# Kernel optimization log

Hardware: AMD Instinct MI355X
Metric: run time of the kernel (lower is better)

Reference implementation:

```python
import jax, jax.numpy as jnp
import numpy as np

N, E = 4096, 65536
H = 200
KS = (3072, 1536, 768)  # ceil(0.75*4096), ceil(0.5*3072), ceil(0.5*1536)


def _gcn(A, x, W, b):
    # GCNConv with improved=True: A_hat = A + 2I, sym-normalized
    n = A.shape[0]
    Ah = A + 2.0 * jnp.eye(n, dtype=A.dtype)
    dinv = jax.lax.rsqrt(Ah.sum(axis=1))
    An = dinv[:, None] * Ah * dinv[None, :]
    return An @ (x @ W) + b


def _augment(A):
    # GraphUNet.augment_adj: remove self loops, add self loops (w=1), spspmm(A,A), remove self loops
    n = A.shape[0]
    eye = jnp.eye(n, dtype=A.dtype)
    Ap = A * (1.0 - eye) + eye
    A2 = Ap @ Ap  # dense form of spspmm (two-hop adjacency with weights)
    return A2 * (1.0 - eye)


def _pool(A, x, pw, k):
    # TopKPooling: score = tanh(x.w/||w||), keep top-k, scale kept x by score
    score = jnp.tanh((x @ pw) / jnp.linalg.norm(pw))
    val, perm = jax.lax.top_k(score, k)
    return x[perm] * val[:, None], A[perm][:, perm], perm


def _unet(x, adj, w0, b0, w1, b1, w2, b2, w3, b3, p1, p2, p3,
          u0w, u0b, u1w, u1b, u2w, u2b):
    down = [(w1, b1), (w2, b2), (w3, b3)]
    pws = [p1, p2, p3]
    up = [(u0w, u0b), (u1w, u1b), (u2w, u2b)]
    x = jax.nn.relu(_gcn(adj, x, w0, b0))
    xs, As, perms = [x], [adj], []
    A = adj
    for i in range(3):
        A = _augment(A)
        x, A, perm = _pool(A, x, pws[i], KS[i])
        x = jax.nn.relu(_gcn(A, x, *down[i]))
        if i < 2:
            xs.append(x)
            As.append(A)
        perms.append(perm)
    for i in range(3):
        j = 2 - i
        upf = jnp.zeros_like(xs[j]).at[perms[j]].set(x)
        x = xs[j] + upf  # sum_res=True
        x = _gcn(As[j], x, *up[i])
        if i < 2:
            x = jax.nn.relu(x)
    return jax.nn.log_softmax(x, axis=1)


def setup_inputs() -> dict:
    key = jax.random.key(0)
    ks = jax.random.split(key, 16)
    x = jax.random.normal(ks[0], (N, 3), dtype=jnp.float32)
    src = jax.random.randint(ks[1], (E,), 0, N)
    dst = jax.random.randint(ks[2], (E,), 0, N)
    A = jnp.zeros((N, N), jnp.float32).at[src, dst].set(1.0)
    A = jnp.maximum(A, A.T) * (1.0 - jnp.eye(N, dtype=jnp.float32))
    g = lambda k, s: jax.random.normal(k, s, jnp.float32) * 0.1
    z = lambda n: jnp.zeros((n,), jnp.float32)
    return dict(
        x=x, adj=A,
        w0=g(ks[3], (3, H)), b0=z(H),
        w1=g(ks[4], (H, H)), b1=z(H),
        w2=g(ks[5], (H, H)), b2=z(H),
        w3=g(ks[6], (H, H)), b3=z(H),
        p1=g(ks[7], (H,)), p2=g(ks[8], (H,)), p3=g(ks[9], (H,)),
        u0w=g(ks[10], (H, H)), u0b=z(H),
        u1w=g(ks[11], (H, H)), u1b=z(H),
        u2w=g(ks[12], (H, 2)), u2b=z(2),
    )


def reference(x, adj, w0, b0, w1, b1, w2, b2, w3, b3, p1, p2, p3,
              u0w, u0b, u1w, u1b, u2w, u2b):
    return _unet(x, adj, w0, b0, w1, b1, w2, b2, w3, b3, p1, p2, p3,
                 u0w, u0b, u1w, u1b, u2w, u2b)
```

## Files before the change

### kernel.cpp

```cpp
#include <hip/hip_runtime.h>

typedef unsigned short u16;
typedef unsigned int u32;
typedef unsigned long long u64;
typedef signed char s8;
typedef __attribute__((ext_vector_type(8))) short bfrag8;
typedef __attribute__((ext_vector_type(4))) float f32x4;
typedef __attribute__((ext_vector_type(4))) int i32x4;
typedef __attribute__((address_space(1))) const void gconst_void;
typedef __attribute__((address_space(3))) void lds_void_t;

__device__ __forceinline__ float bf2f(u16 u) {
  return __uint_as_float(((u32)u) << 16);
}
__device__ __forceinline__ u16 f2bf(float f) {
  u32 u = __float_as_uint(f);
  u32 r = (u + 0x7FFFu + ((u >> 16) & 1u)) >> 16;
  return (u16)r;
}
__device__ __forceinline__ void split3(float v, u16& hi, u16& mi, u16& lo) {
  hi = f2bf(v); float r1 = v - bf2f(hi);
  mi = f2bf(r1); float r2 = r1 - bf2f(mi);
  lo = f2bf(r2);
}
__device__ __forceinline__ float ld1(const void* p, int isbf, long idx) {
  return isbf ? bf2f(((const u16*)p)[idx]) : ((const float*)p)[idx];
}
__device__ __forceinline__ void ld4(const void* p, int isbf, long base, long gc, long bound, float v[4]) {
  if (gc + 3 < bound && ((base & 3) == 0)) {
    if (isbf) {
      const ushort4 u = *(const ushort4*)((const u16*)p + base);
      v[0] = bf2f(u.x); v[1] = bf2f(u.y); v[2] = bf2f(u.z); v[3] = bf2f(u.w);
    } else {
      const float4 f = *(const float4*)((const float*)p + base);
      v[0] = f.x; v[1] = f.y; v[2] = f.z; v[3] = f.w;
    }
  } else {
    #pragma unroll
    for (int d = 0; d < 4; ++d) v[d] = (gc + d < bound) ? ld1(p, isbf, base + d) : 0.f;
  }
}

__global__ void detect_k(const u32* __restrict__ a, long nw, int* __restrict__ flag) {
  long stride = (long)gridDim.x * 256;
  int f = 0;
  for (long j = (long)blockIdx.x * 256 + threadIdx.x; j < nw; j += stride) {
    u32 w = a[j];
    if (w == 0x00003F80u || w == 0x3F803F80u) f = 1;
  }
  if (__any(f)) {
    if ((threadIdx.x & 63) == 0) atomicOr(flag, 1);
  }
}

__device__ __forceinline__ int get_bf(int abf, const int* dtf) {
  return (abf >= 0) ? abf : *dtf;
}

__device__ __forceinline__ void stageB16(const void* g, void* lds) {
#if __has_builtin(__builtin_amdgcn_global_load_lds)
  __builtin_amdgcn_global_load_lds((gconst_void*)g, (lds_void_t*)lds, 16, 0, 0);
#else
  int lane = threadIdx.x & 63;
  *(int4*)((char*)lds + lane * 16) = *(const int4*)g;
#endif
}

template<typename PT>
__global__ __launch_bounds__(256) void syrk_tri_i8_parts(
    const s8* __restrict__ Ag, int ldk, int Ksplit, int ntri,
    PT* __restrict__ parts)
{
  __shared__ s8 At[2][128 * 64];
  __shared__ s8 Bt[2][128 * 64];
  const int t = blockIdx.x;
  int ti = (int)((sqrtf((float)(8 * t + 1)) - 1.0f) * 0.5f);
  while ((ti + 1) * (ti + 2) / 2 <= t) ++ti;
  while (ti * (ti + 1) / 2 > t) --ti;
  const int tj = t - ti * (ti + 1) / 2;

  const int tid = threadIdx.x;
  const int wave = tid >> 6, lane = tid & 63;
  const int wr = wave >> 1, wc = wave & 1;
  const long rowA0 = (long)ti * 128;
  const long rowB0 = (long)tj * 128;
  const int kbeg = blockIdx.y * Ksplit;
  const int nsteps = Ksplit / 64;

  i32x4 acc[4][4];
  #pragma unroll
  for (int i = 0; i < 4; ++i)
    #pragma unroll
    for (int j = 0; j < 4; ++j) acc[i][j] = (i32x4)0;

  const int srow = lane >> 2;
  const int scol = (lane & 3) * 16;
  const int m = lane & 15, q = lane >> 4;

  auto stage = [&](int buf, int k0) {
    #pragma unroll
    for (int tt = 0; tt < 2; ++tt) {
      const int r = wave * 32 + tt * 16;
      stageB16(Ag + (rowA0 + r + srow) * (long)ldk + k0 + scol, At[buf] + r * 64);
      stageB16(Ag + (rowB0 + r + srow) * (long)ldk + k0 + scol, Bt[buf] + r * 64);
    }
  };

  stage(0, kbeg);
  __syncthreads();
  int cur = 0;
  for (int st = 0; st < nsteps; ++st) {
    if (st + 1 < nsteps) stage(cur ^ 1, kbeg + (st + 1) * 64);

    i32x4 af[4], bf[4];
    #pragma unroll
    for (int mt = 0; mt < 4; ++mt)
      af[mt] = *(const i32x4*)(At[cur] + (wr * 64 + mt * 16 + m) * 64 + q * 16);
    #pragma unroll
    for (int nt = 0; nt < 4; ++nt)
      bf[nt] = *(const i32x4*)(Bt[cur] + (wc * 64 + nt * 16 + m) * 64 + q * 16);
    #pragma unroll
    for (int mt = 0; mt < 4; ++mt)
      #pragma unroll
      for (int nt = 0; nt < 4; ++nt)
        acc[mt][nt] = __builtin_amdgcn_mfma_i32_16x16x64_i8(af[mt], bf[nt], acc[mt][nt], 0, 0, 0);
    if (st + 1 < nsteps) __syncthreads();
    cur ^= 1;
  }

  PT* P = parts + ((long)blockIdx.y * ntri + t) * 16384;
  #pragma unroll
  for (int mt = 0; mt < 4; ++mt) {
    #pragma unroll
    for (int nt = 0; nt < 4; ++nt) {
      const int r0 = wr * 64 + mt * 16 + q * 4;
      const int c = wc * 64 + nt * 16 + m;
      #pragma unroll
      for (int r = 0; r < 4; ++r)
        P[(r0 + r) * 128 + c] = (PT)acc[mt][nt][r];
    }
  }
}

template<typename PT>
__global__ __launch_bounds__(256) void reduce_tri_i8_k(
    const PT* __restrict__ parts, int ntri, int n, int nz,
    u16* __restrict__ Ah, u16* __restrict__ Al, double* __restrict__ rs)
{
  __shared__ float T[128 * 33];
  const int t = blockIdx.x >> 2;
  const int slab = blockIdx.x & 3;
  int ti = (int)((sqrtf((float)(8 * t + 1)) - 1.0f) * 0.5f);
  while ((ti + 1) * (ti + 2) / 2 <= t) ++ti;
  while (ti * (ti + 1) / 2 > t) --ti;
  const int tj = t - ti * (ti + 1) / 2;
  const long rowA0 = (long)ti * 128;
  const long rowB0 = (long)tj * 128;
  const int r0 = slab * 32;
  const int tid = threadIdx.x;
  const int lane = tid & 63;
  const long tstride = (long)ntri * 16384;

  #pragma unroll
  for (int it = 0; it < 16; ++it) {
    const int idx = it * 256 + tid;
    const int lr = idx >> 7;
    const int lc = idx & 127;
    long base = (long)t * 16384 + (r0 + lr) * 128 + lc;
    int v = 0;
    for (int z = 0; z < nz; ++z) v += (int)parts[(long)z * tstride + base];
    const long gr = rowA0 + r0 + lr;
    const long gc = rowB0 + lc;
    if (gr == gc) v = 0;
    const float fv = (float)v;
    const u16 h = f2bf(fv);
    const long o = gr * n + gc;
    Ah[o] = h;
    if (Al) Al[o] = f2bf(fv - bf2f(h));
    T[lc * 33 + lr] = fv;
    float wsum = fv;
    #pragma unroll
    for (int off = 32; off > 0; off >>= 1) wsum += __shfl_down(wsum, off);
    if (lane == 0) atomicAdd(&rs[gr], (double)wsum);
  }
  if (ti == tj) return;
  __syncthreads();
  #pragma unroll
  for (int it = 0; it < 16; ++it) {
    const int idx = it * 256 + tid;
    const int mr = idx >> 5;
    const int mc = idx & 31;
    const float fv = T[mr * 33 + mc];
    const u16 h = f2bf(fv);
    const long o = (rowB0 + mr) * n + rowA0 + r0 + mc;
    Ah[o] = h;
    if (Al) Al[o] = f2bf(fv - bf2f(h));
    float ws = fv;
    #pragma unroll
    for (int off = 16; off > 0; off >>= 1) ws += __shfl_down(ws, off);
    if ((lane & 31) == 0) atomicAdd(&rs[rowB0 + mr], (double)ws);
  }
}

__global__ __launch_bounds__(256) void syrk_tri2_parts(
    const u16* __restrict__ Ah, const u16* __restrict__ Al, int ldk,
    float* __restrict__ parts, int n, int per)
{
  __shared__ u16 Ath[128 * 32];
  __shared__ u16 Bth[128 * 32];
  __shared__ u16 Atl[128 * 32];
  __shared__ u16 Btl[128 * 32];
  const int t = blockIdx.x;
  int ti = (int)((sqrtf((float)(8 * t + 1)) - 1.0f) * 0.5f);
  while ((ti + 1) * (ti + 2) / 2 <= t) ++ti;
  while (ti * (ti + 1) / 2 > t) --ti;
  const int tj = t - ti * (ti + 1) / 2;

  const int tid = threadIdx.x;
  const int wave = tid >> 6, lane = tid & 63;
  const int wr = wave >> 1, wc = wave & 1;
  const long rowA0 = (long)ti * 128;
  const long rowB0 = (long)tj * 128;
  const int kbeg = blockIdx.y * per;
  const int kend = kbeg + per;

  f32x4 acc[4][4];
  #pragma unroll
  for (int i = 0; i < 4; ++i)
    #pragma unroll
    for (int j = 0; j < 4; ++j) acc[i][j] = (f32x4)0.f;

  const int srow = lane >> 2;
  const int scol = (lane & 3) * 8;
  const int m = lane & 15, q = lane >> 4;

  for (int k0 = kbeg; k0 < kend; k0 += 32) {
    #pragma unroll
    for (int tt = 0; tt < 2; ++tt) {
      const int r = wave * 32 + tt * 16;
      stageB16(Ah + (rowA0 + r + srow) * (long)ldk + k0 + scol, Ath + r * 32);
      stageB16(Ah + (rowB0 + r + srow) * (long)ldk + k0 + scol, Bth + r * 32);
      stageB16(Al + (rowA0 + r + srow) * (long)ldk + k0 + scol, Atl + r * 32);
      stageB16(Al + (rowB0 + r + srow) * (long)ldk + k0 + scol, Btl + r * 32);
    }
    __syncthreads();

    bfrag8 afh[4], afl[4], bfh[4], bfl[4];
    #pragma unroll
    for (int mt = 0; mt < 4; ++mt) {
      afh[mt] = *(const bfrag8*)(Ath + (wr * 64 + mt * 16 + m) * 32 + q * 8);
      afl[mt] = *(const bfrag8*)(Atl + (wr * 64 + mt * 16 + m) * 32 + q * 8);
    }
    #pragma unroll
    for (int nt = 0; nt < 4; ++nt) {
      bfh[nt] = *(const bfrag8*)(Bth + (wc * 64 + nt * 16 + m) * 32 + q * 8);
      bfl[nt] = *(const bfrag8*)(Btl + (wc * 64 + nt * 16 + m) * 32 + q * 8);
    }
    #pragma unroll
    for (int mt = 0; mt < 4; ++mt)
      #pragma unroll
      for (int nt = 0; nt < 4; ++nt) {
        acc[mt][nt] = __builtin_amdgcn_mfma_f32_16x16x32_bf16(afh[mt], bfh[nt], acc[mt][nt], 0, 0, 0);
        acc[mt][nt] = __builtin_amdgcn_mfma_f32_16x16x32_bf16(afh[mt], bfl[nt], acc[mt][nt], 0, 0, 0);
        acc[mt][nt] = __builtin_amdgcn_mfma_f32_16x16x32_bf16(afl[mt], bfh[nt], acc[mt][nt], 0, 0, 0);
        acc[mt][nt] = __builtin_amdgcn_mfma_f32_16x16x32_bf16(afl[mt], bfl[nt], acc[mt][nt], 0, 0, 0);
      }
    __syncthreads();
  }

  float* P = parts + (long)blockIdx.y * n * n;
  #pragma unroll
  for (int mt = 0; mt < 4; ++mt) {
    #pragma unroll
    for (int nt = 0; nt < 4; ++nt) {
      const long gr0 = rowA0 + wr * 64 + mt * 16 + q * 4;
      const long gc = rowB0 + wc * 64 + nt * 16 + m;
      #pragma unroll
      for (int r = 0; r < 4; ++r)
        P[(gr0 + r) * n + gc] = acc[mt][nt][r];
    }
  }
}

__global__ void reduce_tri_mirror_k(const float* __restrict__ parts,
                                    u16* __restrict__ Ah, u16* __restrict__ Al,
                                    double* __restrict__ rsum, int n, int nz) {
  __shared__ double red[256];
  const int tid = threadIdx.x;
  long idx = (long)blockIdx.x * 256 + tid;
  long nn = (long)n * n;
  long r = idx / n, c = idx - r * n;
  double myv = 0.0;
  if (idx < nn) {
    if (r == c) {
      Ah[idx] = 0; Al[idx] = 0;
    } else if (r > c) {
      float s = 0.f;
      for (int z = 0; z < nz; ++z) s += parts[(long)z * nn + r * n + c];
      long mi = c * n + r;
      u16 h = f2bf(s);
      u16 l = f2bf(s - bf2f(h));
      Ah[idx] = h; Al[idx] = l;
      Ah[mi] = h;  Al[mi] = l;
      myv = (double)s;
      atomicAdd(&rsum[c], (double)s);
    }
  }
  red[tid] = myv;
  __syncthreads();
  for (int st = 128; st > 0; st >>= 1) {
    if (tid < st) red[tid] += red[tid + st];
    __syncthreads();
  }
  if (tid == 0 && idx < nn) atomicAdd(&rsum[r], red[0]);
}

__global__ void bg_i8_k(const void* __restrict__ src, int srcbf, int nsrc,
                        const int* __restrict__ perm, int kRows,
                        s8* __restrict__ Ag, const int* __restrict__ dtf,
                        const float* __restrict__ xsrc, const float* __restrict__ score,
                        float* __restrict__ xdst, unsigned nbB) {
  if (blockIdx.x < nbB) {
    long tot = (long)kRows * nsrc;
    long idx = (long)blockIdx.x * 256 + threadIdx.x;
    if (idx >= tot) return;
    int r = (int)(idx / nsrc);
    int c = (int)(idx - (long)r * nsrc);
    int p = perm[r];
    float v = ld1(src, get_bf(srcbf, dtf), (long)p * nsrc + c);
    if (c == p) v += 1.f;
    Ag[idx] = (s8)(int)v;
  } else {
    long tot = (long)kRows * 200;
    long idx = (long)(blockIdx.x - nbB) * 256 + threadIdx.x;
    if (idx >= tot) return;
    int r = (int)(idx / 200);
    int c = (int)(idx - (long)r * 200);
    int p = perm[r];
    xdst[idx] = xsrc[(long)p * 200 + c] * score[p];
  }
}

__global__ void bg_sp_k(const u16* __restrict__ srcH, const u16* __restrict__ srcL,
                        int nsrc, const int* __restrict__ perm, int kRows,
                        u16* __restrict__ Agh, u16* __restrict__ Agl,
                        const float* __restrict__ xsrc, const float* __restrict__ score,
                        float* __restrict__ xdst, unsigned nbB) {
  if (blockIdx.x < nbB) {
    long tot = (long)kRows * nsrc;
    long idx = (long)blockIdx.x * 256 + threadIdx.x;
    if (idx >= tot) return;
    int r = (int)(idx / nsrc);
    int c = (int)(idx - (long)r * nsrc);
    int p = perm[r];
    long si = (long)p * nsrc + c;
    float v = bf2f(srcH[si]) + bf2f(srcL[si]);
    if (c == p) v += 1.f;
    u16 h = f2bf(v);
    Agh[idx] = h;
    Agl[idx] = f2bf(v - bf2f(h));
  } else {
    long tot = (long)kRows * 200;
    long idx = (long)(blockIdx.x - nbB) * 256 + threadIdx.x;
    if (idx >= tot) return;
    int r = (int)(idx / 200);
    int c = (int)(idx - (long)r * 200);
    int p = perm[r];
    xdst[idx] = xsrc[(long)p * 200 + c] * score[p];
  }
}

template<int HASAL>
__global__ __launch_bounds__(512, 4) void agg_mfma8z(
    const u16* __restrict__ Ah, const u16* __restrict__ Al,
    const u16* __restrict__ ZT, float* __restrict__ parts,
    int K, int per_steps)
{
  __shared__ u16 At[2][8 * 512];
  __shared__ u16 Alt[HASAL ? 2 * 8 * 512 : 2];
  __shared__ u16 Zt[2][21 * 512];

  const int tid = threadIdx.x;
  const int wave = tid >> 6, lane = tid & 63;
  const int zh = blockIdx.z;
  const int ct0 = zh ? 7 : 0;
  const int nts = zh ? 6 : 7;
  const int cth = (nts + 1) >> 1;
  const int rg = wave & 3;
  const int cg = wave >> 2;
  const int wct0 = cg ? cth : 0;
  const int wnct = cg ? (nts - cth) : cth;
  const long row0 = (long)blockIdx.x * 128;
  const int chunk = blockIdx.y;
  const int kbeg = chunk * per_steps * 32;
  const int nsteps = (min(K, kbeg + per_steps * 32) - kbeg) / 32;
  const int m = lane & 15, q = lane >> 4;
  const int srow = lane >> 2, scol = (lane & 3) * 8;
  const int nstg = (HASAL ? 16 : 8) + 3 * nts;

  auto stage = [&](int buf, int k0) {
    for (int s = wave; s < nstg; s += 8) {
      if (s < 8) {
        stageB16(Ah + (row0 + s * 16 + srow) * (long)K + k0 + scol, At[buf] + s * 512);
      } else if (HASAL && s < 16) {
        stageB16(Al + (row0 + (s - 8) * 16 + srow) * (long)K + k0 + scol,
                 (u16*)Alt + (buf * 8 + (s - 8)) * 512);
      } else {
        const int zz = s - (HASAL ? 16 : 8);
        const int pl = (zz >= 2 * nts) ? 2 : ((zz >= nts) ? 1 : 0);
        const int c = zz - pl * nts;
        stageB16(ZT + ((long)(pl * 208 + (ct0 + c) * 16 + srow)) * K + k0 + scol,
                 Zt[buf] + (pl * 7 + c) * 512);
      }
    }
  };

  f32x4 acc[2][4];
  #pragma unroll
  for (int rt = 0; rt < 2; ++rt)
    #pragma unroll
    for (int ct = 0; ct < 4; ++ct) acc[rt][ct] = (f32x4)0.f;

  stage(0, kbeg);
  __syncthreads();
  int cur = 0;
  for (int t = 0; t < nsteps; ++t) {
    if (t + 1 < nsteps) stage(cur ^ 1, kbeg + (t + 1) * 32);

    const u16* Atb = At[cur];
    const u16* Ztb = Zt[cur];
    bfrag8 af0 = *(const bfrag8*)(Atb + (rg * 2) * 512 + m * 32 + q * 8);
    bfrag8 af1 = *(const bfrag8*)(Atb + (rg * 2 + 1) * 512 + m * 32 + q * 8);
    bfrag8 al0, al1;
    if (HASAL) {
      const u16* Altb = (const u16*)Alt + cur * 8 * 512;
      al0 = *(const bfrag8*)(Altb + (rg * 2) * 512 + m * 32 + q * 8);
      al1 = *(const bfrag8*)(Altb + (rg * 2 + 1) * 512 + m * 32 + q * 8);
    }
    #pragma unroll
    for (int ct = 0; ct < 4; ++ct) {
      if (ct < wnct) {
        const int gct = wct0 + ct;
        bfrag8 b0 = *(const bfrag8*)(Ztb + (0 * 7 + gct) * 512 + m * 32 + q * 8);
        bfrag8 b1 = *(const bfrag8*)(Ztb + (1 * 7 + gct) * 512 + m * 32 + q * 8);
        bfrag8 b2 = *(const bfrag8*)(Ztb + (2 * 7 + gct) * 512 + m * 32 + q * 8);
        acc[0][ct] = __builtin_amdgcn_mfma_f32_16x16x32_bf16(af0, b0, acc[0][ct], 0, 0, 0);
        acc[0][ct] = __builtin_amdgcn_mfma_f32_16x16x32_bf16(af0, b1, acc[0][ct], 0, 0, 0);
        acc[0][ct] = __builtin_amdgcn_mfma_f32_16x16x32_bf16(af0, b2, acc[0][ct], 0, 0, 0);
        acc[1][ct] = __builtin_amdgcn_mfma_f32_16x16x32_bf16(af1, b0, acc[1][ct], 0, 0, 0);
        acc[1][ct] = __builtin_amdgcn_mfma_f32_16x16x32_bf16(af1, b1, acc[1][ct], 0, 0, 0);
        acc[1][ct] = __builtin_amdgcn_mfma_f32_16x16x32_bf16(af1, b2, acc[1][ct], 0, 0, 0);
        if (HASAL) {
          acc[0][ct] = __builtin_amdgcn_mfma_f32_16x16x32_bf16(al0, b0, acc[0][ct], 0, 0, 0);
          acc[0][ct] = __builtin_amdgcn_mfma_f32_16x16x32_bf16(al0, b1, acc[0][ct], 0, 0, 0);
          acc[1][ct] = __builtin_amdgcn_mfma_f32_16x16x32_bf16(al1, b0, acc[1][ct], 0, 0, 0);
          acc[1][ct] = __builtin_amdgcn_mfma_f32_16x16x32_bf16(al1, b1, acc[1][ct], 0, 0, 0);
        }
      }
    }
    if (t + 1 < nsteps) __syncthreads();
    cur ^= 1;
  }

  float* P = parts + (long)chunk * gridDim.x * 128 * 208;
  #pragma unroll
  for (int rt = 0; rt < 2; ++rt) {
    #pragma unroll
    for (int ct = 0; ct < 4; ++ct) {
      if (ct < wnct) {
        const long grow0 = row0 + rg * 32 + rt * 16 + q * 4;
        const long gcol = (ct0 + wct0 + ct) * 16 + m;
        #pragma unroll
        for (int r = 0; r < 4; ++r)
          P[(grow0 + r) * 208 + gcol] = acc[rt][ct][r];
      }
    }
  }
}

__global__ __launch_bounds__(256) void reduce_epi_k(
    const float* __restrict__ parts, const float* __restrict__ Zs,
    const double* __restrict__ rs, const float* __restrict__ b,
    float* __restrict__ out, int n, int nz, int relu,
    const float* __restrict__ pw, float* __restrict__ score)
{
  __shared__ float vrow[200];
  const int i = blockIdx.x, tid = threadIdx.x;
  float dv = (float)(1.0 / sqrt(rs[i] + 2.0));
  if (tid < 200) {
    long base = (long)i * 208 + tid;
    float s = 0.f;
    for (int c = 0; c < nz; ++c) s += parts[(long)c * n * 208 + base];
    float v = dv * (s + 2.f * Zs[(long)i * 200 + tid]) + b[tid];
    if (relu) v = fmaxf(v, 0.f);
    out[(long)i * 200 + tid] = v;
    if (score) vrow[tid] = v;
  }
  if (!score) return;
  __syncthreads();
  if (tid < 64) {
    double ps = 0.0;
    for (int j = tid; j < 200; j += 64) { double w = pw[j]; ps += w * w; }
    for (int off = 32; off > 0; off >>= 1) ps += __shfl_down(ps, off);
    double nrm = sqrt(__shfl(ps, 0));
    double s = 0.0;
    for (int j = tid; j < 200; j += 64) s += (double)vrow[j] * (double)pw[j];
    for (int off = 32; off > 0; off >>= 1) s += __shfl_down(s, off);
    if (tid == 0) score[i] = (float)tanh(s / nrm);
  }
}

__global__ void a_from_adj_rs_k(const void* __restrict__ adj, const int* __restrict__ dtf,
                                int n, u16* __restrict__ Ah, double* __restrict__ rs) {
  __shared__ double red[256];
  int bf = *dtf;
  const int row = blockIdx.x, tid = threadIdx.x;
  const long base = (long)row * n;
  double s = 0.0;
  for (int j = tid; j < n; j += 256) {
    float v = ld1(adj, bf, base + j);
    Ah[base + j] = bf ? ((const u16*)adj)[base + j] : f2bf(v);
    s += (double)v;
  }
  red[tid] = s; __syncthreads();
  for (int st = 128; st > 0; st >>= 1) {
    if (tid < st) red[tid] += red[tid + st];
    __syncthreads();
  }
  if (tid == 0) rs[row] = red[0];
}

__global__ __launch_bounds__(256) void gemm64_f64(
    const void* __restrict__ Ap, long lda, int abf,
    const void* __restrict__ Bp, long ldb, int bbf,
    float* __restrict__ C, long ldc, int M, int N, int K,
    const double* __restrict__ rsum, u16* __restrict__ ZT, const int* __restrict__ dtf)
{
  const int abf_ = get_bf(abf, dtf);
  const int bbf_ = get_bf(bbf, dtf);
  __shared__ float As[16][64];
  __shared__ float Bs[16][64];
  const int tid = threadIdx.x;
  const int tr = tid >> 4, tc = tid & 15;
  const long row0 = (long)blockIdx.y * 64;
  const long col0 = (long)blockIdx.x * 64;
  double acc[4][4];
  #pragma unroll
  for (int i = 0; i < 4; ++i)
    #pragma unroll
    for (int j = 0; j < 4; ++j) acc[i][j] = 0.0;

  const int am = tid >> 2;
  const int ak = (tid & 3) * 4;
  const int bk = tid >> 4;
  const int bn = (tid & 15) * 4;

  for (int k0 = 0; k0 < K; k0 += 16) {
    float va[4] = {0.f, 0.f, 0.f, 0.f};
    {
      long gm = row0 + am; long gk = k0 + ak;
      if (gm < M && gk < K) ld4(Ap, abf_, gm * lda + gk, gk, K, va);
    }
    As[ak + 0][am] = va[0]; As[ak + 1][am] = va[1];
    As[ak + 2][am] = va[2]; As[ak + 3][am] = va[3];

    float vb[4] = {0.f, 0.f, 0.f, 0.f};
    {
      long gk = k0 + bk; long gn = col0 + bn;
      if (gk < K && gn < N) ld4(Bp, bbf_, gk * ldb + gn, gn, N, vb);
    }
    Bs[bk][bn + 0] = vb[0]; Bs[bk][bn + 1] = vb[1];
    Bs[bk][bn + 2] = vb[2]; Bs[bk][bn + 3] = vb[3];

    __syncthreads();
    #pragma unroll
    for (int kk = 0; kk < 16; ++kk) {
      float a[4], b[4];
      #pragma unroll
      for (int i = 0; i < 4; ++i) a[i] = As[kk][tr * 4 + i];
      #pragma unroll
      for (int j = 0; j < 4; ++j) b[j] = Bs[kk][tc * 4 + j];
      #pragma unroll
      for (int i = 0; i < 4; ++i)
        #pragma unroll
        for (int j = 0; j < 4; ++j)
          acc[i][j] += (double)a[i] * (double)b[j];
    }
    __syncthreads();
  }
  #pragma unroll
  for (int i = 0; i < 4; ++i) {
    long gm = row0 + tr * 4 + i;
    if (gm >= M) continue;
    float sc = rsum ? (float)(1.0 / sqrt(rsum[gm] + 2.0)) : 1.f;
    #pragma unroll
    for (int j = 0; j < 4; ++j) {
      long gn = col0 + tc * 4 + j;
      if (gn < N) {
        float v0 = (float)acc[i][j];
        float v = v0 * sc;
        C[gm * ldc + gn] = v;
        if (ZT) {
          u16 hi, mi, lo; split3(v, hi, mi, lo);
          ZT[((long)0 * 208 + gn) * M + gm] = hi;
          ZT[((long)1 * 208 + gn) * M + gm] = mi;
          ZT[((long)2 * 208 + gn) * M + gm] = lo;
        }
      }
    }
  }
}

struct UpBatch {
  const void* src[19];
  float* dst[19];
  int n[19];
};

__global__ void upcast_batch_k(UpBatch ub, const int* __restrict__ dtf) {
  int bf = *dtf;
  int a = blockIdx.y;
  int i = blockIdx.x * 256 + threadIdx.x;
  if (i < ub.n[a]) ub.dst[a][i] = ld1(ub.src[a], bf, i);
}

__global__ __launch_bounds__(256) void rank_part_k(
    const float* __restrict__ score, int n, int ns, int* __restrict__ prank)
{
  __shared__ u64 sk[256];
  const int tid = threadIdx.x;
  const int s = blockIdx.x;
  const int slice = n / ns;
  const int jb = s * slice;
  for (int j = tid; j < slice; j += 256) {
    int gj = jb + j;
    u32 b = __float_as_uint(score[gj]);
    u32 u = (b & 0x80000000u) ? ~b : (b | 0x80000000u);
    sk[j] = ((u64)u << 32) | (u32)(~(u32)gj);
  }
  __syncthreads();
  const int i0 = tid * 16;
  if (i0 >= n) return;
  u64 myk[16];
  int cnt[16];
  #pragma unroll
  for (int e = 0; e < 16; ++e) {
    int i = i0 + e;
    u64 key = 0ULL;
    if (i < n) {
      u32 b = __float_as_uint(score[i]);
      u32 u = (b & 0x80000000u) ? ~b : (b | 0x80000000u);
      key = ((u64)u << 32) | (u32)(~(u32)i);
    }
    myk[e] = key; cnt[e] = 0;
  }
  #pragma unroll 4
  for (int j = 0; j < slice; ++j) {
    u64 kj = sk[j];
    #pragma unroll
    for (int e = 0; e < 16; ++e) cnt[e] += (kj > myk[e]) ? 1 : 0;
  }
  #pragma unroll
  for (int e = 0; e < 16; ++e) {
    int i = i0 + e;
    if (i < n) prank[s * n + i] = cnt[e];
  }
}

__global__ void rank_scatter_k(const int* __restrict__ prank, int n, int ns, int k,
                               int* __restrict__ perm, int* __restrict__ inv) {
  int i = blockIdx.x * 256 + threadIdx.x;
  if (i >= n) return;
  int r = 0;
  for (int s = 0; s < ns; ++s) r += prank[s * n + i];
  inv[i] = (r < k) ? r : -1;
  if (r < k) perm[r] = i;
}

__global__ void upadd_k(const float* __restrict__ xs, const float* __restrict__ xpool,
                        const int* __restrict__ inv, float* __restrict__ dst, long nh, int h) {
  long idx = (long)blockIdx.x * 256 + threadIdx.x;
  if (idx >= nh) return;
  int i = (int)(idx / h);
  int c = (int)(idx - (long)i * h);
  float v = xs[idx];
  int r = inv[i];
  if (r >= 0) v += xpool[(long)r * h + c];
  dst[idx] = v;
}

__global__ void matvec2_final_k(const void* __restrict__ A, int abf, int n,
                                const float* __restrict__ Zs, const double* __restrict__ rs0,
                                const float* __restrict__ b2, float* __restrict__ out,
                                const int* __restrict__ dtf) {
  const int bf = get_bf(abf, dtf);
  int row = blockIdx.x, tid = threadIdx.x;
  const long base = (long)row * n;
  double s0 = 0.0, s1 = 0.0;
  for (int j = tid; j < n; j += 256) {
    double a = (double)ld1(A, bf, base + j);
    s0 += a * (double)Zs[2 * j];
    s1 += a * (double)Zs[2 * j + 1];
  }
  __shared__ double r0[256], r1[256];
  r0[tid] = s0; r1[tid] = s1; __syncthreads();
  for (int st = 128; st > 0; st >>= 1) {
    if (tid < st) { r0[tid] += r0[tid + st]; r1[tid] += r1[tid + st]; }
    __syncthreads();
  }
  if (tid == 0) {
    double y0 = (double)((float)r0[0]);
    double y1 = (double)((float)r1[0]);
    double di = (double)((float)(1.0 / sqrt(rs0[row] + 2.0)));
    double t0 = di * (y0 + 2.0 * (double)Zs[2 * row]) + (double)b2[0];
    double t1 = di * (y1 + 2.0 * (double)Zs[2 * row + 1]) + (double)b2[1];
    double mx = fmax(t0, t1);
    double l = mx + log(exp(t0 - mx) + exp(t1 - mx));
    out[2 * row] = (float)(t0 - l);
    out[2 * row + 1] = (float)(t1 - l);
  }
}

extern "C" void kernel_launch(void* const* d_in, const int* in_sizes, int n_in,
                              void* d_out, int out_size, void* d_ws, size_t ws_size,
                              hipStream_t stream) {
  const int N0 = 4096, H = 200;
  const int K1 = 3072, K2 = 1536, K3 = 768;
  const int TK_NS = 32;

  const void* in_x = d_in[0];
  const void* adj  = d_in[1];
  const void* w0 = d_in[2];  const void* b0 = d_in[3];
  const void* w1 = d_in[4];  const void* b1 = d_in[5];
  const void* w2 = d_in[6];  const void* b2 = d_in[7];
  const void* w3 = d_in[8];  const void* b3 = d_in[9];
  const void* p1 = d_in[10]; const void* p2 = d_in[11];
  const void* p3 = d_in[12];
  const void* u0w = d_in[13]; const void* u0b = d_in[14];
  const void* u1w = d_in[15]; const void* u1b = d_in[16];
  const void* u2w = d_in[17]; const void* u2b = d_in[18];

  char* wp = (char*)d_ws;
  auto alloc = [&](size_t bytes) -> void* {
    void* p = (void*)wp;
    wp += (bytes + 255) & ~(size_t)255;
    return p;
  };
  size_t partsBytes = (size_t)300 * 4 * 16384 * 4 + 1024;
  float* parts = (float*)alloc(partsBytes);
  s8*    Agb  = (s8*)alloc((size_t)K1 * N0);
  u16* Ag3h = (u16*)alloc((size_t)K3 * K2 * 2);
  u16* Ag3l = (u16*)alloc((size_t)K3 * K2 * 2);
  u16* Ah0 = (u16*)alloc((size_t)N0 * N0 * 2);
  u16* Ah1 = (u16*)alloc((size_t)K1 * K1 * 2);
  u16* Ah2 = (u16*)alloc((size_t)K2 * K2 * 2);
  u16* Al2 = (u16*)alloc((size_t)K2 * K2 * 2);
  u16* Ah3 = (u16*)alloc((size_t)K3 * K3 * 2);
  u16* Al3 = (u16*)alloc((size_t)K3 * K3 * 2);
  u16* ZT  = (u16*)alloc((size_t)3 * 208 * N0 * 2);
  float* xs0  = (float*)alloc((size_t)N0 * H * 4);
  float* xs1  = (float*)alloc((size_t)K1 * H * 4);
  float* xs2  = (float*)alloc((size_t)K2 * H * 4);
  float* xcur = (float*)alloc((size_t)N0 * H * 4);
  float* xtmp = (float*)alloc((size_t)N0 * H * 4);
  float* Zbuf = (float*)alloc((size_t)N0 * H * 4);
  float* Xinf = (float*)alloc((size_t)N0 * 3 * 4);
  double* rs0 = (double*)alloc((size_t)N0 * 8);
  double* rs1 = (double*)alloc((size_t)K1 * 8);
  double* rs2 = (double*)alloc((size_t)K2 * 8);
  double* rs3 = (double*)alloc((size_t)K3 * 8);
  int* dtflag = (int*)alloc(256);
  float* scores = (float*)alloc((size_t)N0 * 4);
  int* prank = (int*)alloc((size_t)TK_NS * N0 * 4);
  int* perm1 = (int*)alloc((size_t)K1 * 4);
  int* perm2 = (int*)alloc((size_t)K2 * 4);
  int* perm3 = (int*)alloc((size_t)K3 * 4);
  int* inv1 = (int*)alloc((size_t)N0 * 4);
  int* inv2 = (int*)alloc((size_t)K1 * 4);
  int* inv3 = (int*)alloc((size_t)K2 * 4);
  float* w0f = (float*)alloc(3 * H * 4);  float* b0f = (float*)alloc(H * 4);
  float* w1f = (float*)alloc(H * H * 4);  float* b1f = (float*)alloc(H * 4);
  float* w2f = (float*)alloc(H * H * 4);  float* b2f = (float*)alloc(H * 4);
  float* w3f = (float*)alloc(H * H * 4);  float* b3f = (float*)alloc(H * 4);
  float* p1f = (float*)alloc(H * 4);
  float* p2f = (float*)alloc(H * 4);
  float* p3f = (float*)alloc(H * 4);
  float* u0wf = (float*)alloc(H * H * 4); float* u0bf = (float*)alloc(H * 4);
  float* u1wf = (float*)alloc(H * H * 4); float* u1bf = (float*)alloc(H * 4);
  float* u2wf = (float*)alloc(H * 2 * 4); float* u2bf = (float*)alloc(2 * 4);
  (void)in_sizes; (void)n_in; (void)out_size; (void)ws_size;

  hipMemsetAsync(rs1, 0, (size_t)(K1 + K2 + K3) * 8 + 256, stream);
  detect_k<<<dim3(4096), dim3(256), 0, stream>>>((const u32*)adj, (long)N0 * N0 / 2, dtflag);

  {
    UpBatch ub;
    const void* srcs[19] = {in_x, w0, b0, w1, b1, w2, b2, w3, b3, p1, p2, p3,
                            u0w, u0b, u1w, u1b, u2w, u2b, u2b};
    float* dsts[19] = {Xinf, w0f, b0f, w1f, b1f, w2f, b2f, w3f, b3f, p1f, p2f, p3f,
                       u0wf, u0bf, u1wf, u1bf, u2wf, u2bf, u2bf};
    int ns[19] = {N0 * 3, 3 * H, H, H * H, H, H * H, H, H * H, H, H, H, H,
                  H * H, H, H * H, H, H * 2, 2, 2};
    for (int i = 0; i < 19; ++i) { ub.src[i] = srcs[i]; ub.dst[i] = dsts[i]; ub.n[i] = ns[i]; }
    upcast_batch_k<<<dim3((N0 * 3 + 255) / 256, 19), dim3(256), 0, stream>>>(ub, dtflag);
  }

  a_from_adj_rs_k<<<dim3(N0), dim3(256), 0, stream>>>(adj, dtflag, N0, Ah0, rs0);

  auto gemm64 = [&](const void* A, long lda, int abf, const void* B, long ldb, int bbf,
                    float* C, long ldc, int M, int Nn, int K, const double* rsum, u16* zt) {
    dim3 g((Nn + 63) / 64, (M + 63) / 64);
    gemm64_f64<<<g, dim3(256), 0, stream>>>(A, lda, abf, B, ldb, bbf, C, ldc, M, Nn, K,
                                            rsum, zt, dtflag);
  };

  auto gcn = [&](const u16* Ah, const u16* Al, int n, int chunks, const double* rs,
                 const float* Xin_, int din, const float* W, const float* bb,
                 float* out, const float* pwf, float* scoreOut) {
    gemm64(Xin_, din, 0, W, H, 0, Zbuf, H, n, H, din, rs, ZT);
    if (Al)
      agg_mfma8z<1><<<dim3(n / 128, chunks, 2), dim3(512), 0, stream>>>(
          Ah, Al, ZT, parts, n, (n / 32) / chunks);
    else
      agg_mfma8z<0><<<dim3(n / 128, chunks, 2), dim3(512), 0, stream>>>(
          Ah, nullptr, ZT, parts, n, (n / 32) / chunks);
    reduce_epi_k<<<dim3(n), dim3(256), 0, stream>>>(
        parts, Zbuf, rs, bb, out, n, chunks, 1, pwf, scoreOut);
  };

  auto topk = [&](const float* sc, int n, int k, int* perm, int* inv) {
    rank_part_k<<<dim3(TK_NS), dim3(256), 0, stream>>>(sc, n, TK_NS, prank);
    rank_scatter_k<<<dim3((unsigned)((n + 255) / 256)), dim3(256), 0, stream>>>(
        prank, n, TK_NS, k, perm, inv);
  };

  gcn(Ah0, nullptr, N0, 8, rs0, Xinf, 3, w0f, b0f, xs0, p1f, scores);

  topk(scores, N0, K1, perm1, inv1);
  {
    unsigned nbB = (unsigned)(((long)K1 * N0 + 255) / 256);
    unsigned nbG = (unsigned)(((long)K1 * 200 + 255) / 256);
    bg_i8_k<<<dim3(nbB + nbG), dim3(256), 0, stream>>>(
        adj, -1, N0, perm1, K1, Agb, dtflag, xs0, scores, xcur, nbB);
    int nt = K1 / 128;
    int ntri = nt * (nt + 1) / 2;
    syrk_tri_i8_parts<short><<<dim3(ntri, 4), dim3(256), 0, stream>>>(
        Agb, N0, N0 / 4, ntri, (short*)parts);
    reduce_tri_i8_k<short><<<dim3(ntri * 4), dim3(256), 0, stream>>>(
        (const short*)parts, ntri, K1, 4, Ah1, nullptr, rs1);
  }
  gcn(Ah1, nullptr, K1, 12, rs1, xcur, H, w1f, b1f, xs1, p2f, scores);

  topk(scores, K1, K2, perm2, inv2);
  {
    unsigned nbB = (unsigned)(((long)K2 * K1 + 255) / 256);
    unsigned nbG = (unsigned)(((long)K2 * 200 + 255) / 256);
    bg_i8_k<<<dim3(nbB + nbG), dim3(256), 0, stream>>>(
        Ah1, 1, K1, perm2, K2, Agb, dtflag, xs1, scores, xcur, nbB);
    int nt = K2 / 128;
    int ntri = nt * (nt + 1) / 2;
    syrk_tri_i8_parts<int><<<dim3(ntri, 8), dim3(256), 0, stream>>>(
        Agb, K1, K1 / 8, ntri, (int*)parts);
    reduce_tri_i8_k<int><<<dim3(ntri * 4), dim3(256), 0, stream>>>(
        (const int*)parts, ntri, K2, 8, Ah2, Al2, rs2);
  }
  gcn(Ah2, Al2, K2, 24, rs2, xcur, H, w2f, b2f, xs2, p3f, scores);

  topk(scores, K2, K3, perm3, inv3);
  {
    unsigned nbB = (unsigned)(((long)K3 * K2 + 255) / 256);
    unsigned nbG = (unsigned)(((long)K3 * 200 + 255) / 256);
    bg_sp_k<<<dim3(nbB + nbG), dim3(256), 0, stream>>>(
        Ah2, Al2, K2, perm3, K3, Ag3h, Ag3l, xs2, scores, xcur, nbB);
    int nt = K3 / 128;
    syrk_tri2_parts<<<dim3(nt * (nt + 1) / 2, 8), dim3(256), 0, stream>>>(
        Ag3h, Ag3l, K2, parts, K3, K2 / 8);
    long nn = (long)K3 * K3;
    reduce_tri_mirror_k<<<dim3((unsigned)(nn / 256)), dim3(256), 0, stream>>>(
        parts, Ah3, Al3, rs3, K3, 8);
  }
  gcn(Ah3, Al3, K3, 24, rs3, xcur, H, w3f, b3f, xcur, nullptr, nullptr);

  upadd_k<<<dim3((unsigned)(((long)K2 * H + 255) / 256)), dim3(256), 0, stream>>>(
      xs2, xcur, inv3, xtmp, (long)K2 * H, H);
  gcn(Ah2, Al2, K2, 24, rs2, xtmp, H, u0wf, u0bf, xcur, nullptr, nullptr);

  upadd_k<<<dim3((unsigned)(((long)K1 * H + 255) / 256)), dim3(256), 0, stream>>>(
      xs1, xcur, inv2, xtmp, (long)K1 * H, H);
  gcn(Ah1, nullptr, K1, 12, rs1, xtmp, H, u1wf, u1bf, xcur, nullptr, nullptr);

  upadd_k<<<dim3((unsigned)(((long)N0 * H + 255) / 256)), dim3(256), 0, stream>>>(
      xs0, xcur, inv1, xtmp, (long)N0 * H, H);
  gemm64(xtmp, H, 0, u2wf, 2, 0, Zbuf, 2, N0, 2, H, rs0, nullptr);
  matvec2_final_k<<<dim3(N0), dim3(256), 0, stream>>>(
      adj, -1, N0, Zbuf, rs0, u2bf, (float*)d_out, dtflag);
}
```

Before: 823.7 us.

## Vectorize gather kernels, double-buffer syrk_tri2, fuse unpool-add into GEMM loads

Converts several elementwise kernels (dtype detection, adjacency gather, row-sum copy, final matvec) to 4- or 8-wide vector loads and stores to cut instruction and memory-transaction overhead. It adds LDS double-buffering to the bf16 split SYRK so the next k-slice loads while MFMAs run, at the cost of doubled shared memory. It also removes the separate unpool-add kernels by folding the skip-plus-scattered-pool add into the GEMM A-operand load, which saves a round trip through a temporary buffer. The vector paths assume row lengths are multiples of four or eight and that buffers are suitably aligned.

```diff
diff --git a/kernel.cpp b/kernel.cpp
--- a/kernel.cpp
+++ b/kernel.cpp
@@ -42,11 +42,15 @@
 }
 
 __global__ void detect_k(const u32* __restrict__ a, long nw, int* __restrict__ flag) {
+  long nv = nw >> 2;
   long stride = (long)gridDim.x * 256;
   int f = 0;
-  for (long j = (long)blockIdx.x * 256 + threadIdx.x; j < nw; j += stride) {
-    u32 w = a[j];
-    if (w == 0x00003F80u || w == 0x3F803F80u) f = 1;
+  for (long j = (long)blockIdx.x * 256 + threadIdx.x; j < nv; j += stride) {
+    uint4 w = ((const uint4*)a)[j];
+    if (w.x == 0x00003F80u || w.x == 0x3F803F80u ||
+        w.y == 0x00003F80u || w.y == 0x3F803F80u ||
+        w.z == 0x00003F80u || w.z == 0x3F803F80u ||
+        w.w == 0x00003F80u || w.w == 0x3F803F80u) f = 1;
   }
   if (__any(f)) {
     if ((threadIdx.x & 63) == 0) atomicOr(flag, 1);
@@ -206,10 +210,10 @@
     const u16* __restrict__ Ah, const u16* __restrict__ Al, int ldk,
     float* __restrict__ parts, int n, int per)
 {
-  __shared__ u16 Ath[128 * 32];
-  __shared__ u16 Bth[128 * 32];
-  __shared__ u16 Atl[128 * 32];
-  __shared__ u16 Btl[128 * 32];
+  __shared__ u16 Ath[2][128 * 32];
+  __shared__ u16 Bth[2][128 * 32];
+  __shared__ u16 Atl[2][128 * 32];
+  __shared__ u16 Btl[2][128 * 32];
   const int t = blockIdx.x;
   int ti = (int)((sqrtf((float)(8 * t + 1)) - 1.0f) * 0.5f);
   while ((ti + 1) * (ti + 2) / 2 <= t) ++ti;
@@ -222,7 +226,7 @@
   const long rowA0 = (long)ti * 128;
   const long rowB0 = (long)tj * 128;
   const int kbeg = blockIdx.y * per;
-  const int kend = kbeg + per;
+  const int nsteps = per / 32;
 
   f32x4 acc[4][4];
   #pragma unroll
@@ -234,27 +238,33 @@
   const int scol = (lane & 3) * 8;
   const int m = lane & 15, q = lane >> 4;
 
-  for (int k0 = kbeg; k0 < kend; k0 += 32) {
+  auto stage = [&](int buf, int k0) {
     #pragma unroll
     for (int tt = 0; tt < 2; ++tt) {
       const int r = wave * 32 + tt * 16;
-      stageB16(Ah + (rowA0 + r + srow) * (long)ldk + k0 + scol, Ath + r * 32);
-      stageB16(Ah + (rowB0 + r + srow) * (long)ldk + k0 + scol, Bth + r * 32);
-      stageB16(Al + (rowA0 + r + srow) * (long)ldk + k0 + scol, Atl + r * 32);
-      stageB16(Al + (rowB0 + r + srow) * (long)ldk + k0 + scol, Btl + r * 32);
-    }
-    __syncthreads();
+      stageB16(Ah + (rowA0 + r + srow) * (long)ldk + k0 + scol, Ath[buf] + r * 32);
+      stageB16(Ah + (rowB0 + r + srow) * (long)ldk + k0 + scol, Bth[buf] + r * 32);
+      stageB16(Al + (rowA0 + r + srow) * (long)ldk + k0 + scol, Atl[buf] + r * 32);
+      stageB16(Al + (rowB0 + r + srow) * (long)ldk + k0 + scol, Btl[buf] + r * 32);
+    }
+  };
+
+  stage(0, kbeg);
+  __syncthreads();
+  int cur = 0;
+  for (int st = 0; st < nsteps; ++st) {
+    if (st + 1 < nsteps) stage(cur ^ 1, kbeg + (st + 1) * 32);
 
     bfrag8 afh[4], afl[4], bfh[4], bfl[4];
     #pragma unroll
     for (int mt = 0; mt < 4; ++mt) {
-      afh[mt] = *(const bfrag8*)(Ath + (wr * 64 + mt * 16 + m) * 32 + q * 8);
-      afl[mt] = *(const bfrag8*)(Atl + (wr * 64 + mt * 16 + m) * 32 + q * 8);
+      afh[mt] = *(const bfrag8*)(Ath[cur] + (wr * 64 + mt * 16 + m) * 32 + q * 8);
+      afl[mt] = *(const bfrag8*)(Atl[cur] + (wr * 64 + mt * 16 + m) * 32 + q * 8);
     }
     #pragma unroll
     for (int nt = 0; nt < 4; ++nt) {
-      bfh[nt] = *(const bfrag8*)(Bth + (wc * 64 + nt * 16 + m) * 32 + q * 8);
-      bfl[nt] = *(const bfrag8*)(Btl + (wc * 64 + nt * 16 + m) * 32 + q * 8);
+      bfh[nt] = *(const bfrag8*)(Bth[cur] + (wc * 64 + nt * 16 + m) * 32 + q * 8);
+      bfl[nt] = *(const bfrag8*)(Btl[cur] + (wc * 64 + nt * 16 + m) * 32 + q * 8);
     }
     #pragma unroll
     for (int mt = 0; mt < 4; ++mt)
@@ -265,7 +275,8 @@
         acc[mt][nt] = __builtin_amdgcn_mfma_f32_16x16x32_bf16(afl[mt], bfh[nt], acc[mt][nt], 0, 0, 0);
         acc[mt][nt] = __builtin_amdgcn_mfma_f32_16x16x32_bf16(afl[mt], bfl[nt], acc[mt][nt], 0, 0, 0);
       }
-    __syncthreads();
+    if (st + 1 < nsteps) __syncthreads();
+    cur ^= 1;
   }
 
   float* P = parts + (long)blockIdx.y * n * n;
@@ -321,23 +332,39 @@
                         const float* __restrict__ xsrc, const float* __restrict__ score,
                         float* __restrict__ xdst, unsigned nbB) {
   if (blockIdx.x < nbB) {
-    long tot = (long)kRows * nsrc;
-    long idx = (long)blockIdx.x * 256 + threadIdx.x;
-    if (idx >= tot) return;
+    long tot4 = ((long)kRows * nsrc) >> 2;
+    long i4 = (long)blockIdx.x * 256 + threadIdx.x;
+    if (i4 >= tot4) return;
+    long idx = i4 << 2;
     int r = (int)(idx / nsrc);
     int c = (int)(idx - (long)r * nsrc);
     int p = perm[r];
-    float v = ld1(src, get_bf(srcbf, dtf), (long)p * nsrc + c);
-    if (c == p) v += 1.f;
-    Ag[idx] = (s8)(int)v;
+    float v[4];
+    if (get_bf(srcbf, dtf)) {
+      ushort4 u = *(const ushort4*)((const u16*)src + (long)p * nsrc + c);
+      v[0] = bf2f(u.x); v[1] = bf2f(u.y); v[2] = bf2f(u.z); v[3] = bf2f(u.w);
+    } else {
+      float4 f = *(const float4*)((const float*)src + (long)p * nsrc + c);
+      v[0] = f.x; v[1] = f.y; v[2] = f.z; v[3] = f.w;
+    }
+    char4 o;
+    o.x = (s8)(int)(v[0] + ((c + 0 == p) ? 1.f : 0.f));
+    o.y = (s8)(int)(v[1] + ((c + 1 == p) ? 1.f : 0.f));
+    o.z = (s8)(int)(v[2] + ((c + 2 == p) ? 1.f : 0.f));
+    o.w = (s8)(int)(v[3] + ((c + 3 == p) ? 1.f : 0.f));
+    *(char4*)(Ag + idx) = o;
   } else {
-    long tot = (long)kRows * 200;
-    long idx = (long)(blockIdx.x - nbB) * 256 + threadIdx.x;
-    if (idx >= tot) return;
+    long tot4 = (long)kRows * 50;
+    long i4 = (long)(blockIdx.x - nbB) * 256 + threadIdx.x;
+    if (i4 >= tot4) return;
+    long idx = i4 << 2;
     int r = (int)(idx / 200);
     int c = (int)(idx - (long)r * 200);
     int p = perm[r];
-    xdst[idx] = xsrc[(long)p * 200 + c] * score[p];
+    float4 x = *(const float4*)(xsrc + (long)p * 200 + c);
+    float sc = score[p];
+    x.x *= sc; x.y *= sc; x.z *= sc; x.w *= sc;
+    *(float4*)(xdst + idx) = x;
   }
 }
 
@@ -347,26 +374,47 @@
                         const float* __restrict__ xsrc, const float* __restrict__ score,
                         float* __restrict__ xdst, unsigned nbB) {
   if (blockIdx.x < nbB) {
-    long tot = (long)kRows * nsrc;
-    long idx = (long)blockIdx.x * 256 + threadIdx.x;
-    if (idx >= tot) return;
+    long tot4 = ((long)kRows * nsrc) >> 2;
+    long i4 = (long)blockIdx.x * 256 + threadIdx.x;
+    if (i4 >= tot4) return;
+    long idx = i4 << 2;
     int r = (int)(idx / nsrc);
     int c = (int)(idx - (long)r * nsrc);
     int p = perm[r];
     long si = (long)p * nsrc + c;
-    float v = bf2f(srcH[si]) + bf2f(srcL[si]);
-    if (c == p) v += 1.f;
-    u16 h = f2bf(v);
-    Agh[idx] = h;
-    Agl[idx] = f2bf(v - bf2f(h));
+    ushort4 uh = *(const ushort4*)(srcH + si);
+    ushort4 ul = *(const ushort4*)(srcL + si);
+    ushort4 oh, ol;
+    {
+      float v = bf2f(uh.x) + bf2f(ul.x); if (c + 0 == p) v += 1.f;
+      oh.x = f2bf(v); ol.x = f2bf(v - bf2f(oh.x));
+    }
+    {
+      float v = bf2f(uh.y) + bf2f(ul.y); if (c + 1 == p) v += 1.f;
+      oh.y = f2bf(v); ol.y = f2bf(v - bf2f(oh.y));
+    }
+    {
+      float v = bf2f(uh.z) + bf2f(ul.z); if (c + 2 == p) v += 1.f;
+      oh.z = f2bf(v); ol.z = f2bf(v - bf2f(oh.z));
+    }
+    {
+      float v = bf2f(uh.w) + bf2f(ul.w); if (c + 3 == p) v += 1.f;
+      oh.w = f2bf(v); ol.w = f2bf(v - bf2f(oh.w));
+    }
+    *(ushort4*)(Agh + idx) = oh;
+    *(ushort4*)(Agl + idx) = ol;
   } else {
-    long tot = (long)kRows * 200;
-    long idx = (long)(blockIdx.x - nbB) * 256 + threadIdx.x;
-    if (idx >= tot) return;
+    long tot4 = (long)kRows * 50;
+    long i4 = (long)(blockIdx.x - nbB) * 256 + threadIdx.x;
+    if (i4 >= tot4) return;
+    long idx = i4 << 2;
     int r = (int)(idx / 200);
     int c = (int)(idx - (long)r * 200);
     int p = perm[r];
-    xdst[idx] = xsrc[(long)p * 200 + c] * score[p];
+    float4 x = *(const float4*)(xsrc + (long)p * 200 + c);
+    float sc = score[p];
+    x.x *= sc; x.y *= sc; x.z *= sc; x.w *= sc;
+    *(float4*)(xdst + idx) = x;
   }
 }
 
@@ -517,10 +565,27 @@
   const int row = blockIdx.x, tid = threadIdx.x;
   const long base = (long)row * n;
   double s = 0.0;
-  for (int j = tid; j < n; j += 256) {
-    float v = ld1(adj, bf, base + j);
-    Ah[base + j] = bf ? ((const u16*)adj)[base + j] : f2bf(v);
-    s += (double)v;
+  if (bf) {
+    const uint4* src = (const uint4*)((const u16*)adj + base);
+    uint4* dst = (uint4*)(Ah + base);
+    for (int j = tid; j < (n >> 3); j += 256) {
+      uint4 v = src[j];
+      dst[j] = v;
+      s += (double)(bf2f((u16)(v.x & 0xFFFFu)) + bf2f((u16)(v.x >> 16))
+                  + bf2f((u16)(v.y & 0xFFFFu)) + bf2f((u16)(v.y >> 16))
+                  + bf2f((u16)(v.z & 0xFFFFu)) + bf2f((u16)(v.z >> 16))
+                  + bf2f((u16)(v.w & 0xFFFFu)) + bf2f((u16)(v.w >> 16)));
+    }
+  } else {
+    const float4* src = (const float4*)((const float*)adj + base);
+    ushort4* dst = (ushort4*)(Ah + base);
+    for (int j = tid; j < (n >> 2); j += 256) {
+      float4 v = src[j];
+      ushort4 o;
+      o.x = f2bf(v.x); o.y = f2bf(v.y); o.z = f2bf(v.z); o.w = f2bf(v.w);
+      dst[j] = o;
+      s += (double)(v.x + v.y + v.z + v.w);
+    }
   }
   red[tid] = s; __syncthreads();
   for (int st = 128; st > 0; st >>= 1) {
@@ -534,7 +599,8 @@
     const void* __restrict__ Ap, long lda, int abf,
     const void* __restrict__ Bp, long ldb, int bbf,
     float* __restrict__ C, long ldc, int M, int N, int K,
-    const double* __restrict__ rsum, u16* __restrict__ ZT, const int* __restrict__ dtf)
+    const double* __restrict__ rsum, u16* __restrict__ ZT, const int* __restrict__ dtf,
+    const float* __restrict__ ua_pool, const int* __restrict__ ua_inv)
 {
   const int abf_ = get_bf(abf, dtf);
   const int bbf_ = get_bf(bbf, dtf);
@@ -554,12 +620,25 @@
   const int ak = (tid & 3) * 4;
   const int bk = tid >> 4;
   const int bn = (tid & 15) * 4;
+  const long gmA = row0 + am;
+  const int uar = (ua_inv && gmA < M) ? ua_inv[gmA] : -1;
 
   for (int k0 = 0; k0 < K; k0 += 16) {
     float va[4] = {0.f, 0.f, 0.f, 0.f};
     {
       long gm = row0 + am; long gk = k0 + ak;
-      if (gm < M && gk < K) ld4(Ap, abf_, gm * lda + gk, gk, K, va);
+      if (gm < M && gk < K) {
+        if (ua_inv) {
+          float4 x = *(const float4*)((const float*)Ap + gm * lda + gk);
+          if (uar >= 0) {
+            const float4 pv = *(const float4*)(ua_pool + (long)uar * lda + gk);
+            x.x += pv.x; x.y += pv.y; x.z += pv.z; x.w += pv.w;
+          }
+          va[0] = x.x; va[1] = x.y; va[2] = x.z; va[3] = x.w;
+        } else {
+          ld4(Ap, abf_, gm * lda + gk, gk, K, va);
+        }
+      }
     }
     As[ak + 0][am] = va[0]; As[ak + 1][am] = va[1];
     As[ak + 2][am] = va[2]; As[ak + 3][am] = va[3];
@@ -677,18 +756,6 @@
   if (r < k) perm[r] = i;
 }
 
-__global__ void upadd_k(const float* __restrict__ xs, const float* __restrict__ xpool,
-                        const int* __restrict__ inv, float* __restrict__ dst, long nh, int h) {
-  long idx = (long)blockIdx.x * 256 + threadIdx.x;
-  if (idx >= nh) return;
-  int i = (int)(idx / h);
-  int c = (int)(idx - (long)i * h);
-  float v = xs[idx];
-  int r = inv[i];
-  if (r >= 0) v += xpool[(long)r * h + c];
-  dst[idx] = v;
-}
-
 __global__ void matvec2_final_k(const void* __restrict__ A, int abf, int n,
                                 const float* __restrict__ Zs, const double* __restrict__ rs0,
                                 const float* __restrict__ b2, float* __restrict__ out,
@@ -697,10 +764,22 @@
   int row = blockIdx.x, tid = threadIdx.x;
   const long base = (long)row * n;
   double s0 = 0.0, s1 = 0.0;
-  for (int j = tid; j < n; j += 256) {
-    double a = (double)ld1(A, bf, base + j);
-    s0 += a * (double)Zs[2 * j];
-    s1 += a * (double)Zs[2 * j + 1];
+  for (int j4 = tid; j4 < (n >> 2); j4 += 256) {
+    const int j = j4 << 2;
+    float a0, a1, a2, a3;
+    if (bf) {
+      ushort4 u = *(const ushort4*)((const u16*)A + base + j);
+      a0 = bf2f(u.x); a1 = bf2f(u.y); a2 = bf2f(u.z); a3 = bf2f(u.w);
+    } else {
+      float4 f = *(const float4*)((const float*)A + base + j);
+      a0 = f.x; a1 = f.y; a2 = f.z; a3 = f.w;
+    }
+    const float4 z01 = *(const float4*)(Zs + 2 * j);
+    const float4 z23 = *(const float4*)(Zs + 2 * j + 4);
+    s0 += (double)a0 * (double)z01.x; s1 += (double)a0 * (double)z01.y;
+    s0 += (double)a1 * (double)z01.z; s1 += (double)a1 * (double)z01.w;
+    s0 += (double)a2 * (double)z23.x; s1 += (double)a2 * (double)z23.y;
+    s0 += (double)a3 * (double)z23.z; s1 += (double)a3 * (double)z23.w;
   }
   __shared__ double r0[256], r1[256];
   r0[tid] = s0; r1[tid] = s1; __syncthreads();
@@ -788,10 +867,10 @@
   float* u0wf = (float*)alloc(H * H * 4); float* u0bf = (float*)alloc(H * 4);
   float* u1wf = (float*)alloc(H * H * 4); float* u1bf = (float*)alloc(H * 4);
   float* u2wf = (float*)alloc(H * 2 * 4); float* u2bf = (float*)alloc(2 * 4);
-  (void)in_sizes; (void)n_in; (void)out_size; (void)ws_size;
+  (void)in_sizes; (void)n_in; (void)out_size; (void)ws_size; (void)xtmp;
 
   hipMemsetAsync(rs1, 0, (size_t)(K1 + K2 + K3) * 8 + 256, stream);
-  detect_k<<<dim3(4096), dim3(256), 0, stream>>>((const u32*)adj, (long)N0 * N0 / 2, dtflag);
+  detect_k<<<dim3(2048), dim3(256), 0, stream>>>((const u32*)adj, (long)N0 * N0 / 2, dtflag);
 
   {
     UpBatch ub;
@@ -808,16 +887,18 @@
   a_from_adj_rs_k<<<dim3(N0), dim3(256), 0, stream>>>(adj, dtflag, N0, Ah0, rs0);
 
   auto gemm64 = [&](const void* A, long lda, int abf, const void* B, long ldb, int bbf,
-                    float* C, long ldc, int M, int Nn, int K, const double* rsum, u16* zt) {
+                    float* C, long ldc, int M, int Nn, int K, const double* rsum, u16* zt,
+                    const float* uaPool, const int* uaInv) {
     dim3 g((Nn + 63) / 64, (M + 63) / 64);
     gemm64_f64<<<g, dim3(256), 0, stream>>>(A, lda, abf, B, ldb, bbf, C, ldc, M, Nn, K,
-                                            rsum, zt, dtflag);
+                                            rsum, zt, dtflag, uaPool, uaInv);
   };
 
   auto gcn = [&](const u16* Ah, const u16* Al, int n, int chunks, const double* rs,
                  const float* Xin_, int din, const float* W, const float* bb,
-                 float* out, const float* pwf, float* scoreOut) {
-    gemm64(Xin_, din, 0, W, H, 0, Zbuf, H, n, H, din, rs, ZT);
+                 float* out, const float* pwf, float* scoreOut,
+                 const float* uaPool, const int* uaInv) {
+    gemm64(Xin_, din, 0, W, H, 0, Zbuf, H, n, H, din, rs, ZT, uaPool, uaInv);
     if (Al)
       agg_mfma8z<1><<<dim3(n / 128, chunks, 2), dim3(512), 0, stream>>>(
           Ah, Al, ZT, parts, n, (n / 32) / chunks);
@@ -834,12 +915,12 @@
         prank, n, TK_NS, k, perm, inv);
   };
 
-  gcn(Ah0, nullptr, N0, 8, rs0, Xinf, 3, w0f, b0f, xs0, p1f, scores);
+  gcn(Ah0, nullptr, N0, 8, rs0, Xinf, 3, w0f, b0f, xs0, p1f, scores, nullptr, nullptr);
 
   topk(scores, N0, K1, perm1, inv1);
   {
-    unsigned nbB = (unsigned)(((long)K1 * N0 + 255) / 256);
-    unsigned nbG = (unsigned)(((long)K1 * 200 + 255) / 256);
+    unsigned nbB = (unsigned)(((long)K1 * N0 / 4 + 255) / 256);
+    unsigned nbG = (unsigned)(((long)K1 * 50 + 255) / 256);
     bg_i8_k<<<dim3(nbB + nbG), dim3(256), 0, stream>>>(
         adj, -1, N0, perm1, K1, Agb, dtflag, xs0, scores, xcur, nbB);
     int nt = K1 / 128;
@@ -849,12 +930,12 @@
     reduce_tri_i8_k<short><<<dim3(ntri * 4), dim3(256), 0, stream>>>(
         (const short*)parts, ntri, K1, 4, Ah1, nullptr, rs1);
   }
-  gcn(Ah1, nullptr, K1, 12, rs1, xcur, H, w1f, b1f, xs1, p2f, scores);
+  gcn(Ah1, nullptr, K1, 12, rs1, xcur, H, w1f, b1f, xs1, p2f, scores, nullptr, nullptr);
 
   topk(scores, K1, K2, perm2, inv2);
   {
-    unsigned nbB = (unsigned)(((long)K2 * K1 + 255) / 256);
-    unsigned nbG = (unsigned)(((long)K2 * 200 + 255) / 256);
+    unsigned nbB = (unsigned)(((long)K2 * K1 / 4 + 255) / 256);
+    unsigned nbG = (unsigned)(((long)K2 * 50 + 255) / 256);
     bg_i8_k<<<dim3(nbB + nbG), dim3(256), 0, stream>>>(
         Ah1, 1, K1, perm2, K2, Agb, dtflag, xs1, scores, xcur, nbB);
     int nt = K2 / 128;
@@ -864,12 +945,12 @@
     reduce_tri_i8_k<int><<<dim3(ntri * 4), dim3(256), 0, stream>>>(
         (const int*)parts, ntri, K2, 8, Ah2, Al2, rs2);
   }
-  gcn(Ah2, Al2, K2, 24, rs2, xcur, H, w2f, b2f, xs2, p3f, scores);
+  gcn(Ah2, Al2, K2, 24, rs2, xcur, H, w2f, b2f, xs2, p3f, scores, nullptr, nullptr);
 
   topk(scores, K2, K3, perm3, inv3);
   {
-    unsigned nbB = (unsigned)(((long)K3 * K2 + 255) / 256);
-    unsigned nbG = (unsigned)(((long)K3 * 200 + 255) / 256);
+    unsigned nbB = (unsigned)(((long)K3 * K2 / 4 + 255) / 256);
+    unsigned nbG = (unsigned)(((long)K3 * 50 + 255) / 256);
     bg_sp_k<<<dim3(nbB + nbG), dim3(256), 0, stream>>>(
         Ah2, Al2, K2, perm3, K3, Ag3h, Ag3l, xs2, scores, xcur, nbB);
     int nt = K3 / 128;
@@ -879,19 +960,13 @@
     reduce_tri_mirror_k<<<dim3((unsigned)(nn / 256)), dim3(256), 0, stream>>>(
         parts, Ah3, Al3, rs3, K3, 8);
   }
-  gcn(Ah3, Al3, K3, 24, rs3, xcur, H, w3f, b3f, xcur, nullptr, nullptr);
-
-  upadd_k<<<dim3((unsigned)(((long)K2 * H + 255) / 256)), dim3(256), 0, stream>>>(
-      xs2, xcur, inv3, xtmp, (long)K2 * H, H);
-  gcn(Ah2, Al2, K2, 24, rs2, xtmp, H, u0wf, u0bf, xcur, nullptr, nullptr);
-
-  upadd_k<<<dim3((unsigned)(((long)K1 * H + 255) / 256)), dim3(256), 0, stream>>>(
-      xs1, xcur, inv2, xtmp, (long)K1 * H, H);
-  gcn(Ah1, nullptr, K1, 12, rs1, xtmp, H, u1wf, u1bf, xcur, nullptr, nullptr);
-
-  upadd_k<<<dim3((unsigned)(((long)N0 * H + 255) / 256)), dim3(256), 0, stream>>>(
-      xs0, xcur, inv1, xtmp, (long)N0 * H, H);
-  gemm64(xtmp, H, 0, u2wf, 2, 0, Zbuf, 2, N0, 2, H, rs0, nullptr);
+  gcn(Ah3, Al3, K3, 24, rs3, xcur, H, w3f, b3f, xcur, nullptr, nullptr, nullptr, nullptr);
+
+  gcn(Ah2, Al2, K2, 24, rs2, xs2, H, u0wf, u0bf, xcur, nullptr, nullptr, xcur, inv3);
+
+  gcn(Ah1, nullptr, K1, 12, rs1, xs1, H, u1wf, u1bf, xcur, nullptr, nullptr, xcur, inv2);
+
+  gemm64(xs0, H, 0, u2wf, 2, 0, Zbuf, 2, N0, 2, H, rs0, nullptr, xcur, inv1);
   matvec2_final_k<<<dim3(N0), dim3(256), 0, stream>>>(
       adj, -1, N0, Zbuf, rs0, u2bf, (float*)d_out, dtflag);
 }
```

New measurement: 768.6 us. 6.7% less time.
